# Performance work log

Hardware: AMD Instinct MI355X
Metric: run time of the kernel (lower is better)

The kernel has to match this reference:

```python
import jax, jax.numpy as jnp
import numpy as np

E = 1024
H = 16
D = E // H
B = 2
S = 2048


def setup_inputs() -> dict:
    key = jax.random.key(0)
    ks = jax.random.split(key, 12)
    scale = 0.02
    inp = {
        'query': jax.random.normal(ks[0], (B, S, E), dtype=jnp.float32),
        'key':   jax.random.normal(ks[1], (B, S, E), dtype=jnp.float32),
        'value': jax.random.normal(ks[2], (B, S, E), dtype=jnp.float32),
        'mask':  jnp.tril(jnp.ones((S, S), dtype=bool))[None, None],  # causal [1,1,S,S]
        'Wq': jax.random.normal(ks[3], (E, E), dtype=jnp.float32) * scale,
        'bq': jnp.zeros((E,), dtype=jnp.float32),
        'Wk': jax.random.normal(ks[4], (E, E), dtype=jnp.float32) * scale,
        'bk': jnp.zeros((E,), dtype=jnp.float32),
        'Wv': jax.random.normal(ks[5], (E, E), dtype=jnp.float32) * scale,
        'bv': jnp.zeros((E,), dtype=jnp.float32),
        'Wo': jax.random.normal(ks[6], (E, E), dtype=jnp.float32) * scale,
        'bo': jnp.zeros((E,), dtype=jnp.float32),
    }
    return inp


def _split_heads(x):
    b, s, _ = x.shape
    return x.reshape(b, s, H, D).transpose(0, 2, 1, 3)  # [B,H,S,D]


def reference(query, key, value, mask, Wq, bq, Wk, bk, Wv, bv, Wo, bo):
    # Linear projections (torch Linear: x @ W.T + b)
    q = _split_heads(query @ Wq.T + bq)
    k = _split_heads(key @ Wk.T + bk)
    v = _split_heads(value @ Wv.T + bv)
    inv_sqrt_d = jnp.float32(1.0 / np.sqrt(D))
    scores = jnp.einsum('bhqd,bhkd->bhqk', q, k) * inv_sqrt_d
    scores = jnp.where(mask, scores, jnp.float32(-1e9))  # masked_fill(mask==0, -1e9)
    attn = jax.nn.softmax(scores, axis=-1)
    # dropout p=0 in eval -> identity
    out = jnp.einsum('bhqk,bhkd->bhqd', attn, v)
    out = out.transpose(0, 2, 1, 3).reshape(query.shape[0], -1, E)
    out = out @ Wo.T + bo
    return out, attn
```

## Files before the change

### kernel.cpp

```cpp
#include <hip/hip_runtime.h>

#define B_ 2
#define S_ 2048
#define E_ 1024
#define H_ 16
#define D_ 64

typedef __bf16 bf16_t;
typedef __bf16 bf16x8 __attribute__((ext_vector_type(8)));
typedef __bf16 bf16x4 __attribute__((ext_vector_type(4)));
typedef float f32x4 __attribute__((ext_vector_type(4)));

#define OFF_XB   0u
#define OFF_WB   12582912u
#define OFF_QH   16777216u
#define OFF_CTX  29360128u
#define XSZ      4194304u
#define WSZ      1048576u

__device__ __forceinline__ f32x4 mfma16(bf16x8 a, bf16x8 b, f32x4 c) {
  return __builtin_amdgcn_mfma_f32_16x16x32_bf16(a, b, c, 0, 0, 0);
}

__device__ __forceinline__ void gl_lds16(const bf16_t* g, bf16_t* l) {
  __builtin_amdgcn_global_load_lds(
      (const __attribute__((address_space(1))) void*)g,
      (__attribute__((address_space(3))) void*)l, 16, 0, 0);
}

__global__ __launch_bounds__(256) void convert_kernel(
    const float* __restrict__ q, const float* __restrict__ k, const float* __restrict__ v,
    const float* __restrict__ wq, const float* __restrict__ wk,
    const float* __restrict__ wv, const float* __restrict__ wo,
    bf16_t* __restrict__ ws)
{
  const int z = blockIdx.z;
  const float* src;
  bf16_t* dst;
  int n;
  if (z < 3) {
    src = (z == 0) ? q : (z == 1) ? k : v;
    dst = ws + (size_t)z * XSZ;
    n = XSZ;
  } else {
    src = (z == 3) ? wq : (z == 4) ? wk : (z == 5) ? wv : wo;
    dst = ws + OFF_WB + (size_t)(z - 3) * WSZ;
    n = WSZ;
  }
  const int stride = 512 * 256 * 8;
  for (int base = (int)(blockIdx.x * 256 + threadIdx.x) * 8; base < n; base += stride) {
    float4 a = *(const float4*)(src + base);
    float4 b = *(const float4*)(src + base + 4);
    bf16x8 o = { (bf16_t)a.x, (bf16_t)a.y, (bf16_t)a.z, (bf16_t)a.w,
                 (bf16_t)b.x, (bf16_t)b.y, (bf16_t)b.z, (bf16_t)b.w };
    *(bf16x8*)(dst + base) = o;
  }
}

__global__ __launch_bounds__(256) void qkv_gemm_kernel(
    bf16_t* __restrict__ wsb,
    const float* __restrict__ bq, const float* __restrict__ bk, const float* __restrict__ bv)
{
  __shared__ __align__(16) bf16_t sA[128 * 64];
  __shared__ __align__(16) bf16_t sB[128 * 64];

  const int z = blockIdx.z;
  const bf16_t* A  = wsb + (size_t)z * XSZ;
  const bf16_t* Bm = wsb + OFF_WB + (size_t)z * WSZ;
  const float* bias = (z == 0) ? bq : (z == 1) ? bk : bv;
  bf16_t* out = wsb + OFF_QH + (size_t)z * XSZ;

  const int t = threadIdx.x, lane = t & 63, w = t >> 6;
  const int wm = (w >> 1) << 6, wn = (w & 1) << 6;
  const int m0 = blockIdx.x << 7, n0 = blockIdx.y << 7;
  const int l15 = lane & 15, lg = lane >> 4;

  const int r0 = w << 5;
  const int grow = r0 + (lane >> 3);
  const int gcol = (lane & 7) << 3;
  const bf16_t* gA = A + ((size_t)(m0 + grow) << 10) + gcol;
  const bf16_t* gB = Bm + ((size_t)(n0 + grow) << 10) + gcol;
  bf16_t* lA = sA + (r0 << 6);
  bf16_t* lB = sB + (r0 << 6);

  f32x4 acc[4][4] = {};

  for (int k0 = 0; k0 < E_; k0 += 64) {
    __syncthreads();
#pragma unroll
    for (int i = 0; i < 4; ++i) {
      gl_lds16(gA + k0 + ((size_t)(i << 3) << 10), lA + (i << 9));
      gl_lds16(gB + k0 + ((size_t)(i << 3) << 10), lB + (i << 9));
    }
    __syncthreads();
#pragma unroll
    for (int kk = 0; kk < 2; ++kk) {
      bf16x8 af[4], bfr[4];
#pragma unroll
      for (int i = 0; i < 4; ++i)
        af[i] = *(const bf16x8*)(sA + ((wm + (i << 4) + l15) << 6) + (kk << 5) + (lg << 3));
#pragma unroll
      for (int j = 0; j < 4; ++j)
        bfr[j] = *(const bf16x8*)(sB + ((wn + (j << 4) + l15) << 6) + (kk << 5) + (lg << 3));
#pragma unroll
      for (int i = 0; i < 4; ++i)
#pragma unroll
        for (int j = 0; j < 4; ++j)
          acc[i][j] = mfma16(af[i], bfr[j], acc[i][j]);
    }
  }

#pragma unroll
  for (int j = 0; j < 4; ++j) {
    const int n = n0 + wn + (j << 4) + l15;
    const float bn = bias[n];
    const int h = n >> 6, d = n & 63;
#pragma unroll
    for (int i = 0; i < 4; ++i) {
#pragma unroll
      for (int r = 0; r < 4; ++r) {
        const int m = m0 + wm + (i << 4) + (lg << 2) + r;
        const int b = m >> 11, s = m & (S_ - 1);
        out[(((size_t)(b * H_ + h)) * S_ + s) * D_ + d] = (bf16_t)(acc[i][j][r] + bn);
      }
    }
  }
}

__global__ __launch_bounds__(256, 6) void attn_kernel(
    const bf16_t* __restrict__ qh, const bf16_t* __restrict__ kh, const bf16_t* __restrict__ vh,
    float* __restrict__ attn, bf16_t* __restrict__ ctx)
{
  constexpr int STR = 72;
  __shared__ __align__(16) char smem[26624];
  bf16_t* klds  = (bf16_t*)smem;
  bf16_t* vbuf  = (bf16_t*)(smem + 9216);
  bf16_t* plds_ = (bf16_t*)(smem + 17408);
  float*  pf    = (float*)(smem + 9216);

  const int d_  = blockIdx.x;
  const int xcd = d_ & 7;
  const int bh  = (xcd << 2) + ((d_ >> 3) & 3);
  const int qt  = d_ >> 5;

  const int t    = threadIdx.x;
  const int lane = t & 63;
  const int w    = t >> 6;
  const int l15  = lane & 15;
  const int lg   = lane >> 4;
  const int q0 = qt << 6;
  const size_t hbase = (size_t)bh * (size_t)(S_ * D_);

  const int qr_lane = q0 + (w << 4) + l15;
  const bf16_t* qp = qh + hbase + (size_t)qr_lane * D_ + (lg << 3);
  const bf16x8 q_lo = *(const bf16x8*)qp;
  const bf16x8 q_hi = *(const bf16x8*)(qp + 32);

  constexpr float SC = 0.18033688f;

  float s_sum = 0.f;
  f32x4 oacc[4] = {};

  const int td  = t & 63;
  const int tk0 = (t >> 6) << 3;
  const int sr = t >> 3;
  const int sc = (t & 7) << 3;
  const int vtw0 = td * 64 + (tk0 ^ ((td & 7) << 3));
  const int vtw1 = td * 64 + ((tk0 + 32) ^ ((td & 7) << 3));

  for (int kt = 0; kt <= qt; ++kt) {
    __syncthreads();
    {
      const bf16_t* kb = kh + hbase + (size_t)((kt << 6) + sr) * D_ + sc;
      const bf16_t* vb = vh + hbase + (size_t)((kt << 6) + sr) * D_ + sc;
      *(bf16x8*)(klds + sr * STR + sc) = *(const bf16x8*)kb;
      *(bf16x8*)(klds + (sr + 32) * STR + sc) = *(const bf16x8*)(kb + 32 * D_);
      *(bf16x8*)(vbuf + (sr << 6) + sc) = *(const bf16x8*)vb;
      *(bf16x8*)(vbuf + ((sr + 32) << 6) + sc) = *(const bf16x8*)(vb + 32 * D_);
    }
    __syncthreads();
    bf16x8 col0, col1;
#pragma unroll
    for (int e = 0; e < 8; ++e) col0[e] = vbuf[((tk0 + e) << 6) + td];
#pragma unroll
    for (int e = 0; e < 8; ++e) col1[e] = vbuf[((tk0 + 32 + e) << 6) + td];
#pragma unroll
    for (int j = 0; j < 4; ++j) {
      const bf16_t* kp = klds + ((j << 4) + l15) * STR + (lg << 3);
      bf16x8 k_lo = *(const bf16x8*)kp;
      bf16x8 k_hi = *(const bf16x8*)(kp + 32);
      f32x4 sf = { 0.f, 0.f, 0.f, 0.f };
      sf = mfma16(k_lo, q_lo, sf);
      sf = mfma16(k_hi, q_hi, sf);
      const int kc = (kt << 6) + (j << 4) + (lg << 2);
      const int lim = qr_lane - kc;
      bf16x4 pb;
#pragma unroll
      for (int r = 0; r < 4; ++r) {
        const float pv = (r <= lim) ? exp2f(sf[r] * SC) : 0.f;
        s_sum += pv;
        pb[r] = (bf16_t)pv;
      }
      *(bf16x4*)(plds_ + w * 1152 + l15 * STR + (j << 4) + (lg << 2)) = pb;
    }
    __syncthreads();
    *(bf16x8*)(vbuf + vtw0) = col0;
    *(bf16x8*)(vbuf + vtw1) = col1;
    __syncthreads();
#pragma unroll
    for (int kk = 0; kk < 2; ++kk) {
      bf16x8 pa = *(const bf16x8*)(plds_ + w * 1152 + l15 * STR + (kk << 5) + (lg << 3));
#pragma unroll
      for (int db = 0; db < 4; ++db) {
        const int d = (db << 4) + l15;
        const int c = (kk << 5) + (lg << 3);
        bf16x8 vb = *(const bf16x8*)(vbuf + d * 64 + (c ^ ((d & 7) << 3)));
        oacc[db] = mfma16(pa, vb, oacc[db]);
      }
    }
  }

  float s = s_sum;
  s += __shfl_xor(s, 16);
  s += __shfl_xor(s, 32);
  const float inv_s = 1.f / s;

  float rinv[4];
#pragma unroll
  for (int r = 0; r < 4; ++r) rinv[r] = __shfl(inv_s, (lg << 2) + r);

  const int b = bh >> 4, h = bh & 15;
  const int qr_base = q0 + (w << 4) + (lg << 2);
#pragma unroll
  for (int db = 0; db < 4; ++db) {
    const int d = (db << 4) + l15;
#pragma unroll
    for (int r = 0; r < 4; ++r) {
      const int qr = qr_base + r;
      ctx[((size_t)(b * S_ + qr)) * E_ + h * D_ + d] = (bf16_t)(oacc[db][r] * rinv[r]);
    }
  }

  float* attn_bh = attn + (size_t)bh * (size_t)(S_ * S_);
  const int frow = t >> 4;
  const int fcol = (t & 15) << 2;
  for (int kt = 0; kt <= qt; ++kt) {
    __syncthreads();
    {
      const bf16_t* kb = kh + hbase + (size_t)((kt << 6) + sr) * D_ + sc;
      *(bf16x8*)(klds + sr * STR + sc) = *(const bf16x8*)kb;
      *(bf16x8*)(klds + (sr + 32) * STR + sc) = *(const bf16x8*)(kb + 32 * D_);
    }
    __syncthreads();
#pragma unroll
    for (int j = 0; j < 4; ++j) {
      const bf16_t* kp = klds + ((j << 4) + l15) * STR + (lg << 3);
      bf16x8 k_lo = *(const bf16x8*)kp;
      bf16x8 k_hi = *(const bf16x8*)(kp + 32);
      f32x4 sf = { 0.f, 0.f, 0.f, 0.f };
      sf = mfma16(k_lo, q_lo, sf);
      sf = mfma16(k_hi, q_hi, sf);
      const int kc = (kt << 6) + (j << 4) + (lg << 2);
      const int lim = qr_lane - kc;
      f32x4 o;
#pragma unroll
      for (int r = 0; r < 4; ++r)
        o[r] = (r <= lim) ? exp2f(sf[r] * SC) * inv_s : 0.f;
      *(f32x4*)(pf + ((w << 4) + l15) * 68 + (j << 4) + (lg << 2)) = o;
    }
    __syncthreads();
#pragma unroll
    for (int rr = 0; rr < 4; ++rr) {
      const int row = (rr << 4) + frow;
      f32x4 v = *(const f32x4*)(pf + row * 68 + fcol);
      __builtin_nontemporal_store(v,
          (f32x4*)(attn_bh + (size_t)(q0 + row) * S_ + (kt << 6) + fcol));
    }
  }

  const f32x4 fz = { 0.f, 0.f, 0.f, 0.f };
  for (int cb = q0 + 64; cb < S_; cb += 64) {
#pragma unroll
    for (int rr = 0; rr < 4; ++rr) {
      __builtin_nontemporal_store(fz,
          (f32x4*)(attn_bh + (size_t)(q0 + (rr << 4) + frow) * S_ + cb + fcol));
    }
  }
}

__global__ __launch_bounds__(256) void out_gemm_kernel(
    bf16_t* __restrict__ wsb, const float* __restrict__ bo, float* __restrict__ out)
{
  __shared__ __align__(16) bf16_t sA[128 * 64];
  __shared__ __align__(16) bf16_t sB[128 * 64];

  const bf16_t* A  = wsb + OFF_CTX;
  const bf16_t* Bm = wsb + OFF_WB + 3u * WSZ;

  const int t = threadIdx.x, lane = t & 63, w = t >> 6;
  const int wm = (w >> 1) << 6, wn = (w & 1) << 6;
  const int m0 = blockIdx.x << 7, n0 = blockIdx.y << 7;
  const int l15 = lane & 15, lg = lane >> 4;

  const int r0 = w << 5;
  const int grow = r0 + (lane >> 3);
  const int gcol = (lane & 7) << 3;
  const bf16_t* gA = A + ((size_t)(m0 + grow) << 10) + gcol;
  const bf16_t* gB = Bm + ((size_t)(n0 + grow) << 10) + gcol;
  bf16_t* lA = sA + (r0 << 6);
  bf16_t* lB = sB + (r0 << 6);

  f32x4 acc[4][4] = {};

  for (int k0 = 0; k0 < E_; k0 += 64) {
    __syncthreads();
#pragma unroll
    for (int i = 0; i < 4; ++i) {
      gl_lds16(gA + k0 + ((size_t)(i << 3) << 10), lA + (i << 9));
      gl_lds16(gB + k0 + ((size_t)(i << 3) << 10), lB + (i << 9));
    }
    __syncthreads();
#pragma unroll
    for (int kk = 0; kk < 2; ++kk) {
      bf16x8 af[4], bfr[4];
#pragma unroll
      for (int i = 0; i < 4; ++i)
        af[i] = *(const bf16x8*)(sA + ((wm + (i << 4) + l15) << 6) + (kk << 5) + (lg << 3));
#pragma unroll
      for (int j = 0; j < 4; ++j)
        bfr[j] = *(const bf16x8*)(sB + ((wn + (j << 4) + l15) << 6) + (kk << 5) + (lg << 3));
#pragma unroll
      for (int i = 0; i < 4; ++i)
#pragma unroll
        for (int j = 0; j < 4; ++j)
          acc[i][j] = mfma16(af[i], bfr[j], acc[i][j]);
    }
  }

#pragma unroll
  for (int j = 0; j < 4; ++j) {
    const int n = n0 + wn + (j << 4) + l15;
    const float bn = bo[n];
#pragma unroll
    for (int i = 0; i < 4; ++i) {
#pragma unroll
      for (int r = 0; r < 4; ++r) {
        const int m = m0 + wm + (i << 4) + (lg << 2) + r;
        out[(size_t)m * E_ + n] = acc[i][j][r] + bn;
      }
    }
  }
}

extern "C" void kernel_launch(void* const* d_in, const int* in_sizes, int n_in,
                              void* d_out, int out_size, void* d_ws, size_t ws_size,
                              hipStream_t stream) {
  const float* query = (const float*)d_in[0];
  const float* key   = (const float*)d_in[1];
  const float* value = (const float*)d_in[2];
  const float* Wq = (const float*)d_in[4];
  const float* bq = (const float*)d_in[5];
  const float* Wk = (const float*)d_in[6];
  const float* bk = (const float*)d_in[7];
  const float* Wv = (const float*)d_in[8];
  const float* bv = (const float*)d_in[9];
  const float* Wo = (const float*)d_in[10];
  const float* bo = (const float*)d_in[11];

  float* out  = (float*)d_out;
  float* attn = out + (size_t)B_ * S_ * E_;

  bf16_t* wsb = (bf16_t*)d_ws;
  bf16_t* qh  = wsb + OFF_QH;
  bf16_t* kh  = qh + XSZ;
  bf16_t* vh  = kh + XSZ;
  bf16_t* ctx = wsb + OFF_CTX;

  convert_kernel<<<dim3(512, 1, 7), dim3(256), 0, stream>>>(
      query, key, value, Wq, Wk, Wv, Wo, wsb);
  qkv_gemm_kernel<<<dim3(32, 8, 3), dim3(256), 0, stream>>>(wsb, bq, bk, bv);
  attn_kernel<<<dim3(1024), dim3(256), 0, stream>>>(qh, kh, vh, attn, ctx);
  out_gemm_kernel<<<dim3(32, 8), dim3(256), 0, stream>>>(wsb, bo, out);
}
```

Baseline: 220.9 us.

## Interleave zero-fill of masked attention with first pass; use LDS-only barriers

The zero stores for the upper-triangle attention tiles are spread across the iterations of the first key loop instead of running in a separate tail loop. This balances the store traffic against compute in every block. All __syncthreads are replaced by a custom barrier that waits only on lgkmcnt (LDS/scalar memory), not on vmcnt. Outstanding global stores and loads can therefore stay in flight across barriers. This relies on the global loads being consumed before the LDS writes that depend on them, which the compiler's own waitcnt insertion should still handle.

```diff
diff --git a/kernel.cpp b/kernel.cpp
--- a/kernel.cpp
+++ b/kernel.cpp
@@ -26,6 +26,13 @@
   __builtin_amdgcn_global_load_lds(
       (const __attribute__((address_space(1))) void*)g,
       (__attribute__((address_space(3))) void*)l, 16, 0, 0);
+}
+
+__device__ __forceinline__ void bar_lgkm() {
+  __builtin_amdgcn_sched_barrier(0);
+  asm volatile("s_waitcnt lgkmcnt(0)" ::: "memory");
+  __builtin_amdgcn_s_barrier();
+  __builtin_amdgcn_sched_barrier(0);
 }
 
 __global__ __launch_bounds__(256) void convert_kernel(
@@ -168,8 +175,16 @@
   const int vtw0 = td * 64 + (tk0 ^ ((td & 7) << 3));
   const int vtw1 = td * 64 + ((tk0 + 32) ^ ((td & 7) << 3));
 
+  float* attn_bh = attn + (size_t)bh * (size_t)(S_ * S_);
+  const int frow = t >> 4;
+  const int fcol = (t & 15) << 2;
+  const int nfill = 31 - qt;
+  const int iters = qt + 1;
+  int fdone = 0;
+  const f32x4 fz = { 0.f, 0.f, 0.f, 0.f };
+
   for (int kt = 0; kt <= qt; ++kt) {
-    __syncthreads();
+    bar_lgkm();
     {
       const bf16_t* kb = kh + hbase + (size_t)((kt << 6) + sr) * D_ + sc;
       const bf16_t* vb = vh + hbase + (size_t)((kt << 6) + sr) * D_ + sc;
@@ -178,7 +193,7 @@
       *(bf16x8*)(vbuf + (sr << 6) + sc) = *(const bf16x8*)vb;
       *(bf16x8*)(vbuf + ((sr + 32) << 6) + sc) = *(const bf16x8*)(vb + 32 * D_);
     }
-    __syncthreads();
+    bar_lgkm();
     bf16x8 col0, col1;
 #pragma unroll
     for (int e = 0; e < 8; ++e) col0[e] = vbuf[((tk0 + e) << 6) + td];
@@ -203,10 +218,18 @@
       }
       *(bf16x4*)(plds_ + w * 1152 + l15 * STR + (j << 4) + (lg << 2)) = pb;
     }
-    __syncthreads();
+    const int ftarget = (nfill * (kt + 1)) / iters;
+    for (; fdone < ftarget; ++fdone) {
+      const int kcol0 = (qt + 1 + fdone) << 6;
+#pragma unroll
+      for (int rr = 0; rr < 4; ++rr)
+        __builtin_nontemporal_store(fz,
+            (f32x4*)(attn_bh + (size_t)(q0 + (rr << 4) + frow) * S_ + kcol0 + fcol));
+    }
+    bar_lgkm();
     *(bf16x8*)(vbuf + vtw0) = col0;
     *(bf16x8*)(vbuf + vtw1) = col1;
-    __syncthreads();
+    bar_lgkm();
 #pragma unroll
     for (int kk = 0; kk < 2; ++kk) {
       bf16x8 pa = *(const bf16x8*)(plds_ + w * 1152 + l15 * STR + (kk << 5) + (lg << 3));
@@ -241,17 +264,16 @@
     }
   }
 
-  float* attn_bh = attn + (size_t)bh * (size_t)(S_ * S_);
-  const int frow = t >> 4;
-  const int fcol = (t & 15) << 2;
+  const int frow2 = t >> 4;
+  const int fcol2 = (t & 15) << 2;
   for (int kt = 0; kt <= qt; ++kt) {
-    __syncthreads();
+    bar_lgkm();
     {
       const bf16_t* kb = kh + hbase + (size_t)((kt << 6) + sr) * D_ + sc;
       *(bf16x8*)(klds + sr * STR + sc) = *(const bf16x8*)kb;
       *(bf16x8*)(klds + (sr + 32) * STR + sc) = *(const bf16x8*)(kb + 32 * D_);
     }
-    __syncthreads();
+    bar_lgkm();
 #pragma unroll
     for (int j = 0; j < 4; ++j) {
       const bf16_t* kp = klds + ((j << 4) + l15) * STR + (lg << 3);
@@ -268,22 +290,13 @@
         o[r] = (r <= lim) ? exp2f(sf[r] * SC) * inv_s : 0.f;
       *(f32x4*)(pf + ((w << 4) + l15) * 68 + (j << 4) + (lg << 2)) = o;
     }
-    __syncthreads();
+    bar_lgkm();
 #pragma unroll
     for (int rr = 0; rr < 4; ++rr) {
-      const int row = (rr << 4) + frow;
-      f32x4 v = *(const f32x4*)(pf + row * 68 + fcol);
+      const int row = (rr << 4) + frow2;
+      f32x4 v = *(const f32x4*)(pf + row * 68 + fcol2);
       __builtin_nontemporal_store(v,
-          (f32x4*)(attn_bh + (size_t)(q0 + row) * S_ + (kt << 6) + fcol));
-    }
-  }
-
-  const f32x4 fz = { 0.f, 0.f, 0.f, 0.f };
-  for (int cb = q0 + 64; cb < S_; cb += 64) {
-#pragma unroll
-    for (int rr = 0; rr < 4; ++rr) {
-      __builtin_nontemporal_store(fz,
-          (f32x4*)(attn_bh + (size_t)(q0 + (rr << 4) + frow) * S_ + cb + fcol));
+          (f32x4*)(attn_bh + (size_t)(q0 + row) * S_ + (kt << 6) + fcol2));
     }
   }
 }
```

Result: slower. 267.9 us (+21.3%).

## Stream K fragments from global with register prefetch in attn writeout pass

Applied to the files above, without the earlier changes.

The second pass over key tiles, which recomputes probabilities and writes the full attention matrix, no longer stages K through LDS. Each wave now loads its 16-row K fragments directly from global into registers, prefetching the next fragment while the current MFMA and exp run, and synchronises only once per 64-column tile for the transposed store. This removes one barrier and the LDS K staging per tile, at the cost of redundant global (L2) reads across waves and extra registers, so the occupancy hint drops from 6 to 4 blocks.

```diff
diff --git a/kernel.cpp b/kernel.cpp
--- a/kernel.cpp
+++ b/kernel.cpp
@@ -127,7 +127,7 @@
   }
 }
 
-__global__ __launch_bounds__(256, 6) void attn_kernel(
+__global__ __launch_bounds__(256, 4) void attn_kernel(
     const bf16_t* __restrict__ qh, const bf16_t* __restrict__ kh, const bf16_t* __restrict__ vh,
     float* __restrict__ attn, bf16_t* __restrict__ ctx)
 {
@@ -244,37 +244,44 @@
   float* attn_bh = attn + (size_t)bh * (size_t)(S_ * S_);
   const int frow = t >> 4;
   const int fcol = (t & 15) << 2;
-  for (int kt = 0; kt <= qt; ++kt) {
-    __syncthreads();
-    {
-      const bf16_t* kb = kh + hbase + (size_t)((kt << 6) + sr) * D_ + sc;
-      *(bf16x8*)(klds + sr * STR + sc) = *(const bf16x8*)kb;
-      *(bf16x8*)(klds + (sr + 32) * STR + sc) = *(const bf16x8*)(kb + 32 * D_);
-    }
-    __syncthreads();
-#pragma unroll
-    for (int j = 0; j < 4; ++j) {
-      const bf16_t* kp = klds + ((j << 4) + l15) * STR + (lg << 3);
-      bf16x8 k_lo = *(const bf16x8*)kp;
-      bf16x8 k_hi = *(const bf16x8*)(kp + 32);
-      f32x4 sf = { 0.f, 0.f, 0.f, 0.f };
-      sf = mfma16(k_lo, q_lo, sf);
-      sf = mfma16(k_hi, q_hi, sf);
-      const int kc = (kt << 6) + (j << 4) + (lg << 2);
-      const int lim = qr_lane - kc;
-      f32x4 o;
-#pragma unroll
-      for (int r = 0; r < 4; ++r)
-        o[r] = (r <= lim) ? exp2f(sf[r] * SC) * inv_s : 0.f;
-      *(f32x4*)(pf + ((w << 4) + l15) * 68 + (j << 4) + (lg << 2)) = o;
-    }
-    __syncthreads();
-#pragma unroll
-    for (int rr = 0; rr < 4; ++rr) {
-      const int row = (rr << 4) + frow;
-      f32x4 v = *(const f32x4*)(pf + row * 68 + fcol);
-      __builtin_nontemporal_store(v,
-          (f32x4*)(attn_bh + (size_t)(q0 + row) * S_ + (kt << 6) + fcol));
+  __syncthreads();
+
+  const bf16_t* kpB = kh + hbase + (size_t)l15 * D_ + (lg << 3);
+  const int M = (qt + 1) << 2;
+  bf16x8 kc_lo = *(const bf16x8*)kpB;
+  bf16x8 kc_hi = *(const bf16x8*)(kpB + 32);
+
+  for (int m = 0; m < M; ++m) {
+    const int mn = (m + 1 < M) ? (m + 1) : m;
+    const bf16_t* np = kpB + ((size_t)mn << 10);
+    bf16x8 kn_lo = *(const bf16x8*)np;
+    bf16x8 kn_hi = *(const bf16x8*)(np + 32);
+
+    f32x4 sf = { 0.f, 0.f, 0.f, 0.f };
+    sf = mfma16(kc_lo, q_lo, sf);
+    sf = mfma16(kc_hi, q_hi, sf);
+    const int kc = (m << 4) + (lg << 2);
+    const int lim = qr_lane - kc;
+    f32x4 o;
+#pragma unroll
+    for (int r = 0; r < 4; ++r)
+      o[r] = (r <= lim) ? exp2f(sf[r] * SC) * inv_s : 0.f;
+    *(f32x4*)(pf + ((w << 4) + l15) * 68 + ((m & 3) << 4) + (lg << 2)) = o;
+
+    kc_lo = kn_lo;
+    kc_hi = kn_hi;
+
+    if ((m & 3) == 3) {
+      __syncthreads();
+      const int kt = m >> 2;
+#pragma unroll
+      for (int rr = 0; rr < 4; ++rr) {
+        const int row = (rr << 4) + frow;
+        f32x4 v = *(const f32x4*)(pf + row * 68 + fcol);
+        __builtin_nontemporal_store(v,
+            (f32x4*)(attn_bh + (size_t)(q0 + row) * S_ + (kt << 6) + fcol));
+      }
+      __syncthreads();
     }
   }
 
```

Result: slower. 225.3 us (+2.0%).
